# Performance work log

Hardware: AMD Instinct MI355X
Metric: run time of the kernel (lower is better)

## Reference

```python
import jax, jax.numpy as jnp
import numpy as np

HIDDEN = 64
IN_DIM = 32
CONNECTION = 8
N_WARPS = (CONNECTION + 1) // 2  # range(0, connection, 2) -> 4 warps actually used


def conv2d(x, w, b, pad):
    # x: (B, Cin, H, W), w: (Cout, Cin, kh, kw)
    y = jax.lax.conv_general_dilated(
        x, w, window_strides=(1, 1), padding=[(pad, pad), (pad, pad)],
        dimension_numbers=("NCHW", "OIHW", "NCHW"))
    return y + b[None, :, None, None]


def grid_sample_bilinear(img, grid):
    """torch.nn.functional.grid_sample(mode='bilinear', padding_mode='zeros', align_corners=False).
    img: (B, C, H, W); grid: (B, H, W, 2) with grid[..., 0]=x (width), grid[..., 1]=y (height)."""
    B, C, H, W = img.shape
    gx = (grid[..., 0] + 1.0) * (W * 0.5) - 0.5  # unnormalize, align_corners=False
    gy = (grid[..., 1] + 1.0) * (H * 0.5) - 0.5
    x0 = jnp.floor(gx)
    y0 = jnp.floor(gy)
    wx1 = gx - x0
    wy1 = gy - y0
    wx0 = 1.0 - wx1
    wy0 = 1.0 - wy1

    def gather(xf, yf):
        valid = (xf >= 0) & (xf < W) & (yf >= 0) & (yf < H)
        xi = jnp.clip(xf, 0, W - 1).astype(jnp.int32)
        yi = jnp.clip(yf, 0, H - 1).astype(jnp.int32)
        # per-batch advanced gather: (C, H, W) per sample
        v = jax.vmap(lambda im, y, x: im[:, y, x])(img, yi, xi)  # (B, C, H, W)
        return v * valid[:, None, :, :].astype(img.dtype)

    out = (wy0 * wx0)[:, None] * gather(x0, y0) \
        + (wy0 * wx1)[:, None] * gather(x0 + 1, y0) \
        + (wy1 * wx0)[:, None] * gather(x0, y0 + 1) \
        + (wy1 * wx1)[:, None] * gather(x0 + 1, y0 + 1)
    return out


def setup_inputs() -> dict:
    key = jax.random.key(0)
    ks = jax.random.split(key, 10)
    B, H, W = 16, 128, 128
    s = 0.05
    return {
        "x": jax.random.normal(ks[0], (B, IN_DIM, H, W), dtype=jnp.float32),
        "h_prev": jax.random.normal(ks[1], (B, HIDDEN, H, W), dtype=jnp.float32),
        "w_in": jax.random.normal(ks[2], (3 * HIDDEN, IN_DIM, 3, 3), dtype=jnp.float32) * s,
        "b_in": jax.random.normal(ks[3], (3 * HIDDEN,), dtype=jnp.float32) * s,
        "w_proj": jax.random.normal(ks[4], (N_WARPS, 3 * HIDDEN, HIDDEN), dtype=jnp.float32) * s,
        "b_proj": jax.random.normal(ks[5], (N_WARPS, 3 * HIDDEN), dtype=jnp.float32) * s,
        "w_sub": jax.random.normal(ks[6], (2 * CONNECTION, IN_DIM + HIDDEN, 5, 5), dtype=jnp.float32) * s,
        "b_sub": jax.random.normal(ks[7], (2 * CONNECTION,), dtype=jnp.float32) * s,
    }


def reference(x, h_prev, w_in, b_in, w_proj, b_proj, w_sub, b_sub):
    d = HIDDEN
    input_conv = conv2d(x, w_in, b_in, pad=1)  # (B, 3d, H, W)
    x_z, x_r, x_h = input_conv[:, :d], input_conv[:, d:2 * d], input_conv[:, 2 * d:]

    # flow sub-network + global min-max normalization over ALL channels
    combined = jnp.concatenate([x, h_prev], axis=1)
    cc = conv2d(combined, w_sub, b_sub, pad=2)  # (B, 2*connection, H, W)
    cc = jnp.transpose(cc, (0, 2, 3, 1))        # (B, H, W, 2*connection)
    cc = (cc - cc.min()) / (cc.max() - cc.min())
    cc = 2.0 * cc - 1.0

    traj = None
    for i in range(N_WARPS):  # small fixed loop (mirrors range(0, connection, 2))
        grid = cc[..., 2 * i:2 * i + 2]
        warped = grid_sample_bilinear(h_prev, grid)  # (B, d, H, W)
        proj = jnp.einsum("bchw,oc->bohw", warped, w_proj[i]) + b_proj[i][None, :, None, None]
        traj = proj if traj is None else traj + proj

    h_z, h_r, h_h = traj[:, :d], traj[:, d:2 * d], traj[:, 2 * d:]
    z = jax.nn.sigmoid(x_z + h_z)
    r = jax.nn.sigmoid(x_r + h_r)
    h = jax.nn.leaky_relu(x_h + r * h_h, negative_slope=0.2)
    h_next = (1.0 - z) * h + z * h_prev
    return h_next
```

## Files before the change

kernel.cpp:

```cpp
#include <hip/hip_runtime.h>
#include <hip/hip_bf16.h>
#include <math.h>

#define B_    16
#define HID   64
#define CIN   32
#define OC1   192
#define CCC   16
#define HW_   128
#define NPIX  (HW_*HW_)

typedef _Float16 half8 __attribute__((ext_vector_type(8)));
typedef float floatx4 __attribute__((ext_vector_type(4)));

__device__ __forceinline__ unsigned fenc(float f) {
    unsigned b = __float_as_uint(f);
    return (b & 0x80000000u) ? ~b : (b | 0x80000000u);
}
__device__ __forceinline__ float fdec(unsigned u) {
    unsigned b = (u & 0x80000000u) ? (u ^ 0x80000000u) : ~u;
    return __uint_as_float(b);
}

__global__ __launch_bounds__(256) void repack_kernel(
    const float* __restrict__ w_in, const float* __restrict__ w_sub,
    const float* __restrict__ w_proj, const float* __restrict__ b_proj,
    _Float16* __restrict__ wsub_f16, float* __restrict__ bsum,
    _Float16* __restrict__ win_f16, _Float16* __restrict__ wp_f16,
    unsigned* __restrict__ minmax)
{
    int idx = blockIdx.x * 256 + threadIdx.x;
    if (idx < 38400) {
        int sk = idx >> 9, r2 = idx & 511;
        int l = r2 >> 3, j = r2 & 7;
        int s = sk / 3, kc = sk - s * 3;
        int ky = s / 5, kx = s - ky * 5;
        int oc = l & 15;
        int icg = kc * 32 + (l >> 4) * 8 + j;
        wsub_f16[idx] = (_Float16)w_sub[oc * 2400 + icg * 25 + ky * 5 + kx];
    } else if (idx < 38400 + 192) {
        int o = idx - 38400;
        bsum[o] = b_proj[o] + b_proj[192 + o] + b_proj[384 + o] + b_proj[576 + o];
    } else if (idx < 38592 + 55296) {
        int j2 = idx - 38592;
        int s = j2 / 6144, r = j2 - s * 6144;
        int mt = r / 512, r2 = r - mt * 512;
        int l = r2 >> 3, j = r2 & 7;
        int oc = mt * 16 + (l & 15);
        int ic = (l >> 4) * 8 + j;
        win_f16[j2] = (_Float16)w_in[oc * 288 + ic * 9 + s];
    } else if (idx < 38592 + 55296 + 49152) {
        int j3 = idx - (38592 + 55296);
        int kt = j3 / 6144, r = j3 - kt * 6144;
        int mt = r / 512, r2 = r - mt * 512;
        int l = r2 >> 3, j = r2 & 7;
        int o = mt * 16 + (l & 15);
        int c_all = kt * 32 + (l >> 4) * 8 + j;
        int i = c_all >> 6, c = c_all & 63;
        wp_f16[j3] = (_Float16)w_proj[(i * 192 + o) * 64 + c];
    }
    if (idx == 0) { minmax[0] = 0xFFFFFFFFu; minmax[1] = 0u; }
}

__global__ __launch_bounds__(256) void transpose_h_kernel(
    const float* __restrict__ hp, const float* __restrict__ x,
    _Float16* __restrict__ hcl, _Float16* __restrict__ xcl)
{
    __shared__ float lds[64 * 129];
    int tid = threadIdx.x;
    int y = blockIdx.x, b = blockIdx.y;

    const float* hb = hp + (size_t)b * HID * NPIX + y * HW_;
#pragma unroll
    for (int it = 0; it < 32; ++it) {
        int idx = tid + it * 256;
        int c = idx >> 7, xx = idx & 127;
        lds[c * 129 + xx] = hb[(size_t)c * NPIX + xx];
    }
    __syncthreads();
    unsigned* o = (unsigned*)(hcl + (size_t)((b * HW_ + y) * HW_) * 64);
#pragma unroll
    for (int it = 0; it < 16; ++it) {
        int e2 = tid + it * 256;
        int c2 = e2 & 31, xx = e2 >> 5;
        union { _Float16 h[2]; unsigned u; } pk;
        pk.h[0] = (_Float16)lds[(c2 * 2) * 129 + xx];
        pk.h[1] = (_Float16)lds[(c2 * 2 + 1) * 129 + xx];
        o[e2] = pk.u;
    }
    __syncthreads();

    const float* xb = x + (size_t)b * CIN * NPIX + y * HW_;
#pragma unroll
    for (int it = 0; it < 16; ++it) {
        int idx = tid + it * 256;
        int c = idx >> 7, xx = idx & 127;
        lds[c * 129 + xx] = xb[(size_t)c * NPIX + xx];
    }
    __syncthreads();
    unsigned* ox = (unsigned*)(xcl + (size_t)((b * HW_ + y) * HW_) * 32);
#pragma unroll
    for (int it = 0; it < 8; ++it) {
        int e2 = tid + it * 256;
        int c2 = e2 & 15, xx = e2 >> 4;
        union { _Float16 h[2]; unsigned u; } pk;
        pk.h[0] = (_Float16)lds[(c2 * 2) * 129 + xx];
        pk.h[1] = (_Float16)lds[(c2 * 2 + 1) * 129 + xx];
        ox[e2] = pk.u;
    }
}

__global__ __launch_bounds__(256) void conv_sub_mfma(
    const _Float16* __restrict__ xcl, const _Float16* __restrict__ hcl,
    const _Float16* __restrict__ wsub_f16, const float* __restrict__ b_sub,
    float* __restrict__ cc, unsigned* __restrict__ minmax)
{
    __shared__ __align__(16) _Float16 tile[12 * 20 * 104];
    __shared__ float redmn[4], redmx[4];
    int tid = threadIdx.x;
    int b = blockIdx.z;
    int y0 = blockIdx.y * 8, x0 = blockIdx.x * 16;

#pragma unroll
    for (int it = 0; it < 8; ++it) {
        int idx = tid + it * 256;
        if (idx < 1920) {
            int yy = idx / 160, rem = idx - yy * 160;
            int px = rem >> 3, q = rem & 7;
            int gy = y0 + yy - 2, gx = x0 + px - 2;
            bool ok = ((unsigned)gy < 128u) & ((unsigned)gx < 128u);
            int cgy = min(max(gy, 0), 127), cgx = min(max(gx, 0), 127);
            uint4 v = ((const uint4*)hcl)[(size_t)((b * 128 + cgy) * 128 + cgx) * 8 + q];
            if (!ok) { v.x = 0; v.y = 0; v.z = 0; v.w = 0; }
            *(uint4*)((char*)tile + (yy * 20 + px) * 208 + 64 + q * 16) = v;
        }
    }
#pragma unroll
    for (int it = 0; it < 4; ++it) {
        int idx = tid + it * 256;
        if (idx < 960) {
            int yy = idx / 80, rem = idx - yy * 80;
            int px = rem >> 2, q = rem & 3;
            int gy = y0 + yy - 2, gx = x0 + px - 2;
            bool ok = ((unsigned)gy < 128u) & ((unsigned)gx < 128u);
            int cgy = min(max(gy, 0), 127), cgx = min(max(gx, 0), 127);
            uint4 v = ((const uint4*)xcl)[(size_t)((b * 128 + cgy) * 128 + cgx) * 4 + q];
            if (!ok) { v.x = 0; v.y = 0; v.z = 0; v.w = 0; }
            *(uint4*)((char*)tile + (yy * 20 + px) * 208 + q * 16) = v;
        }
    }
    __syncthreads();

    int w = tid >> 6, l = tid & 63;
    int quad = l >> 4, ln = l & 15;

    floatx4 sinit;
#pragma unroll
    for (int r = 0; r < 4; ++r) sinit[r] = b_sub[quad * 4 + r];
    floatx4 sacc[2] = {sinit, sinit};

#pragma unroll 5
    for (int s = 0; s < 25; ++s) {
        int ky = s / 5, kx = s - (s / 5) * 5;
#pragma unroll
        for (int kc = 0; kc < 3; ++kc) {
            half8 af = *(const half8*)(wsub_f16 + (size_t)((s * 3 + kc) * 64 + l) * 8);
#pragma unroll
            for (int t = 0; t < 2; ++t) {
                int pos = (w * 2 + t + ky) * 20 + (ln + kx);
                half8 bf = *(const half8*)(tile + pos * 104 + kc * 32 + quad * 8);
                sacc[t] = __builtin_amdgcn_mfma_f32_16x16x32_f16(af, bf, sacc[t], 0, 0, 0);
            }
        }
    }

    {
        float mn = 1e30f, mx = -1e30f;
#pragma unroll
        for (int t = 0; t < 2; ++t) {
            int yg = y0 + w * 2 + t;
#pragma unroll
            for (int r = 0; r < 4; ++r) {
                int oc = quad * 4 + r;
                float v = sacc[t][r];
                cc[((size_t)(b * CCC + oc) * HW_ + yg) * HW_ + x0 + ln] = v;
                mn = fminf(mn, v); mx = fmaxf(mx, v);
            }
        }
#pragma unroll
        for (int m = 1; m < 64; m <<= 1) {
            mn = fminf(mn, __shfl_xor(mn, m, 64));
            mx = fmaxf(mx, __shfl_xor(mx, m, 64));
        }
        if (l == 0) { redmn[w] = mn; redmx[w] = mx; }
    }
    __syncthreads();
    if (tid == 0) {
        float bmn = fminf(fminf(redmn[0], redmn[1]), fminf(redmn[2], redmn[3]));
        float bmx = fmaxf(fmaxf(redmx[0], redmx[1]), fmaxf(redmx[2], redmx[3]));
        atomicMin(&minmax[0], fenc(bmn));
        atomicMax(&minmax[1], fenc(bmx));
    }
}

__global__ __launch_bounds__(256, 4) void warp_gru_conv(
    const float* __restrict__ hp, const _Float16* __restrict__ hcl,
    const _Float16* __restrict__ xcl, const float* __restrict__ cc,
    const _Float16* __restrict__ wp_f16, const float* __restrict__ bsum,
    const _Float16* __restrict__ win_f16, const float* __restrict__ b_in,
    const unsigned* __restrict__ minmax, float* __restrict__ out)
{
    __shared__ __align__(16) _Float16 smem[64 * 256];
    _Float16* xt = smem;
    _Float16* warped = smem;

    int tid = threadIdx.x;
    int i = tid >> 6;
    int p = tid & 63;
    int b = blockIdx.z, y = blockIdx.y, xh = blockIdx.x;
    int xg = xh * 64 + p;
    int w = i, l = p;
    int quad = l >> 4, ln = l & 15;

    uint4 xv0, xv1, xv2, xv3;
    int xslot = -1;
    if (tid < 216) {
        int row = tid / 72, px = tid - row * 72;
        int gy = y - 1 + row, gx = xh * 64 - 4 + px;
        bool ok = ((unsigned)gy < 128u) & ((unsigned)gx < 128u);
        int cgy = min(max(gy, 0), 127), cgx = min(max(gx, 0), 127);
        const uint4* s = (const uint4*)(xcl + (size_t)((b * 128 + cgy) * 128 + cgx) * 32);
        xv0 = s[0]; xv1 = s[1]; xv2 = s[2]; xv3 = s[3];
        if (!ok) {
            xv0.x = xv0.y = xv0.z = xv0.w = 0; xv1 = xv0; xv2 = xv0; xv3 = xv0;
        }
        xslot = (row * 72 + px) * 4;
    }

    float mn = fdec(minmax[0]), mx = fdec(minmax[1]);
    float scale = 2.0f / (mx - mn);
    int ccbase = ((b * CCC + 2 * i) * HW_ + y) * HW_ + xg;
    float gxn = (cc[ccbase] - mn) * scale - 1.0f;
    float gyn = (cc[ccbase + NPIX] - mn) * scale - 1.0f;
    float gx = (gxn + 1.0f) * 64.0f - 0.5f;
    float gy = (gyn + 1.0f) * 64.0f - 0.5f;
    float x0f = floorf(gx), y0f = floorf(gy);
    float wx1 = gx - x0f, wy1 = gy - y0f;
    float wx0 = 1.0f - wx1, wy0 = 1.0f - wy1;
    int ix0 = (int)x0f, iy0 = (int)y0f;
    int ix1 = ix0 + 1, iy1 = iy0 + 1;
    bool vx0 = (unsigned)ix0 < 128u, vx1 = (unsigned)ix1 < 128u;
    bool vy0 = (unsigned)iy0 < 128u, vy1 = (unsigned)iy1 < 128u;
    _Float16 h00 = (_Float16)((vx0 && vy0) ? wy0 * wx0 : 0.f);
    _Float16 h01 = (_Float16)((vx1 && vy0) ? wy0 * wx1 : 0.f);
    _Float16 h10 = (_Float16)((vx0 && vy1) ? wy1 * wx0 : 0.f);
    _Float16 h11 = (_Float16)((vx1 && vy1) ? wy1 * wx1 : 0.f);
    int cx0 = min(max(ix0, 0), 127), cx1 = min(max(ix1, 0), 127);
    int cy0 = min(max(iy0, 0), 127), cy1 = min(max(iy1, 0), 127);

    const _Float16* hclb = hcl + (size_t)b * NPIX * 64;
    const half8* r00 = (const half8*)(hclb + (size_t)(cy0 * HW_ + cx0) * 64);
    const half8* r01 = (const half8*)(hclb + (size_t)(cy0 * HW_ + cx1) * 64);
    const half8* r10 = (const half8*)(hclb + (size_t)(cy1 * HW_ + cx0) * 64);
    const half8* r11 = (const half8*)(hclb + (size_t)(cy1 * HW_ + cx1) * 64);

    if (xslot >= 0) {
        unsigned b0 = (unsigned)(xslot * 16);
        unsigned by0_ = b0 ^ (((b0 >> 7) & 3) << 4);
        unsigned b1 = (unsigned)((xslot + 1) * 16);
        unsigned by1_ = b1 ^ (((b1 >> 7) & 3) << 4);
        unsigned b2 = (unsigned)((xslot + 2) * 16);
        unsigned by2_ = b2 ^ (((b2 >> 7) & 3) << 4);
        unsigned b3 = (unsigned)((xslot + 3) * 16);
        unsigned by3_ = b3 ^ (((b3 >> 7) & 3) << 4);
        *(uint4*)((char*)xt + by0_) = xv0;
        *(uint4*)((char*)xt + by1_) = xv1;
        *(uint4*)((char*)xt + by2_) = xv2;
        *(uint4*)((char*)xt + by3_) = xv3;
    }
    __syncthreads();

    floatx4 accA[3][4];
    floatx4 hh[4];
#pragma unroll
    for (int t = 0; t < 2; ++t) {
        floatx4 bi = *(const floatx4*)(b_in + t * 64 + 16 * w + quad * 4);
        floatx4 bs = *(const floatx4*)(bsum + t * 64 + 16 * w + quad * 4);
        floatx4 init;
#pragma unroll
        for (int r = 0; r < 4; ++r) init[r] = bi[r] + bs[r];
#pragma unroll
        for (int nt = 0; nt < 4; ++nt) accA[t][nt] = init;
    }
    {
        floatx4 bih = *(const floatx4*)(b_in + 128 + 16 * w + quad * 4);
        floatx4 bsh = *(const floatx4*)(bsum + 128 + 16 * w + quad * 4);
#pragma unroll
        for (int nt = 0; nt < 4; ++nt) { accA[2][nt] = bih; hh[nt] = bsh; }
    }

#pragma unroll
    for (int s = 0; s < 9; ++s) {
        int ky = s / 3, kx = s - ky * 3;
        half8 af[3];
#pragma unroll
        for (int t = 0; t < 3; ++t)
            af[t] = *(const half8*)(win_f16 + (size_t)((s * 12 + (t * 4 + w)) * 64 + l) * 8);
#pragma unroll
        for (int nt = 0; nt < 4; ++nt) {
            int pxr = ky * 72 + nt * 16 + ln + kx + 3;
            unsigned byte = (unsigned)(pxr * 64 + quad * 16);
            byte ^= ((byte >> 7) & 3) << 4;
            half8 bf = *(const half8*)((char*)xt + byte);
#pragma unroll
            for (int t = 0; t < 3; ++t)
                accA[t][nt] = __builtin_amdgcn_mfma_f32_16x16x32_f16(af[t], bf, accA[t][nt], 0, 0, 0);
        }
    }
    __syncthreads();

#pragma unroll
    for (int t = 0; t < 8; ++t) {
        half8 c00 = r00[t], c01 = r01[t], c10 = r10[t], c11 = r11[t];
        half8 v = c00 * h00 + c01 * h01 + c10 * h10 + c11 * h11;
        int cs = (i * 8 + t) ^ (p & 7);
        *(half8*)(warped + p * 256 + cs * 8) = v;
    }
    __syncthreads();

    const float* hb = hp + (size_t)b * HID * NPIX;
    float hpv[4][4];
#pragma unroll
    for (int nt = 0; nt < 4; ++nt) {
#pragma unroll
        for (int r = 0; r < 4; ++r) {
            int d = 16 * w + quad * 4 + r;
            hpv[nt][r] = hb[(size_t)d * NPIX + y * HW_ + xh * 64 + nt * 16 + ln];
        }
    }

#pragma unroll
    for (int kt = 0; kt < 8; ++kt) {
        half8 af[3];
#pragma unroll
        for (int t = 0; t < 3; ++t)
            af[t] = *(const half8*)(wp_f16 + (size_t)((kt * 12 + (t * 4 + w)) * 64 + l) * 8);
#pragma unroll
        for (int nt = 0; nt < 4; ++nt) {
            int pxi = nt * 16 + ln;
            int cs = (kt * 4 + quad) ^ (pxi & 7);
            half8 bf = *(const half8*)(warped + pxi * 256 + cs * 8);
            accA[0][nt] = __builtin_amdgcn_mfma_f32_16x16x32_f16(af[0], bf, accA[0][nt], 0, 0, 0);
            accA[1][nt] = __builtin_amdgcn_mfma_f32_16x16x32_f16(af[1], bf, accA[1][nt], 0, 0, 0);
            hh[nt]      = __builtin_amdgcn_mfma_f32_16x16x32_f16(af[2], bf, hh[nt], 0, 0, 0);
        }
    }

#pragma unroll
    for (int nt = 0; nt < 4; ++nt) {
#pragma unroll
        for (int r = 0; r < 4; ++r) {
            int d = 16 * w + quad * 4 + r;
            int pxi = nt * 16 + ln;
            int pix = y * HW_ + xh * 64 + pxi;
            float z  = 1.0f / (1.0f + __expf(-accA[0][nt][r]));
            float rg = 1.0f / (1.0f + __expf(-accA[1][nt][r]));
            float hc = accA[2][nt][r] + rg * hh[nt][r];
            hc = hc > 0.f ? hc : 0.2f * hc;
            out[(size_t)(b * HID + d) * NPIX + pix] = (1.f - z) * hc + z * hpv[nt][r];
        }
    }
}

extern "C" void kernel_launch(void* const* d_in, const int* in_sizes, int n_in,
                              void* d_out, int out_size, void* d_ws, size_t ws_size,
                              hipStream_t stream)
{
    const float* x      = (const float*)d_in[0];
    const float* hp     = (const float*)d_in[1];
    const float* w_in   = (const float*)d_in[2];
    const float* b_in   = (const float*)d_in[3];
    const float* w_proj = (const float*)d_in[4];
    const float* b_proj = (const float*)d_in[5];
    const float* w_sub  = (const float*)d_in[6];
    const float* b_sub  = (const float*)d_in[7];
    float* out = (float*)d_out;

    char* ws = (char*)d_ws;
    float*     ccbuf    = (float*)    ws;
    unsigned*  minmax   = (unsigned*) (ws + 16777216);
    _Float16*  wsub_f16 = (_Float16*)(ws + 16777472);
    float*     bsum     = (float*)    (ws + 16854272);
    _Float16*  win_f16  = (_Float16*)(ws + 16855296);
    _Float16*  wp_f16   = (_Float16*)(ws + 16965888);
    _Float16*  hcl16    = (_Float16*)(ws + 17064192);
    _Float16*  xcl16    = (_Float16*)(ws + 50618624);

    repack_kernel<<<dim3(559), dim3(256), 0, stream>>>(
        w_in, w_sub, w_proj, b_proj, wsub_f16, bsum, win_f16, wp_f16, minmax);
    transpose_h_kernel<<<dim3(HW_, B_), dim3(256), 0, stream>>>(hp, x, hcl16, xcl16);
    conv_sub_mfma<<<dim3(8, 16, B_), dim3(256), 0, stream>>>(
        xcl16, hcl16, wsub_f16, b_sub, ccbuf, minmax);
    warp_gru_conv<<<dim3(2, HW_, B_), dim3(256), 0, stream>>>(
        hp, hcl16, xcl16, ccbuf, wp_f16, bsum, win_f16, b_in, minmax, out);
}
```

Measured before the change: 393.9 us.

## Stage GRU output through LDS for vectorized stores; read h_prev from fp16 copy

The final GRU kernel now reads h_prev from the fp16 channels-last copy, one half4 per tile, instead of sixteen scalar fp32 loads per thread. It prefetches two of the four bilinear corner rows before the input-conv MFMA loop so their latency overlaps compute. Outputs are staged through padded shared memory and written as float4 along pixels, replacing scattered scalar stores. Launch bounds drop to 3 blocks per CU to make room for the extra registers. This risks lower occupancy, and the blend term z*h_prev now uses an fp16-rounded h_prev, which slightly changes precision.

```diff
diff --git a/kernel.cpp b/kernel.cpp
--- a/kernel.cpp
+++ b/kernel.cpp
@@ -11,6 +11,7 @@
 #define NPIX  (HW_*HW_)
 
 typedef _Float16 half8 __attribute__((ext_vector_type(8)));
+typedef _Float16 half4 __attribute__((ext_vector_type(4)));
 typedef float floatx4 __attribute__((ext_vector_type(4)));
 
 __device__ __forceinline__ unsigned fenc(float f) {
@@ -203,9 +204,9 @@
     }
 }
 
-__global__ __launch_bounds__(256, 4) void warp_gru_conv(
-    const float* __restrict__ hp, const _Float16* __restrict__ hcl,
-    const _Float16* __restrict__ xcl, const float* __restrict__ cc,
+__global__ __launch_bounds__(256, 3) void warp_gru_conv(
+    const _Float16* __restrict__ hcl, const _Float16* __restrict__ xcl,
+    const float* __restrict__ cc,
     const _Float16* __restrict__ wp_f16, const float* __restrict__ bsum,
     const _Float16* __restrict__ win_f16, const float* __restrict__ b_in,
     const unsigned* __restrict__ minmax, float* __restrict__ out)
@@ -213,6 +214,7 @@
     __shared__ __align__(16) _Float16 smem[64 * 256];
     _Float16* xt = smem;
     _Float16* warped = smem;
+    float* ol = (float*)smem;
 
     int tid = threadIdx.x;
     int i = tid >> 6;
@@ -235,6 +237,15 @@
             xv0.x = xv0.y = xv0.z = xv0.w = 0; xv1 = xv0; xv2 = xv0; xv3 = xv0;
         }
         xslot = (row * 72 + px) * 4;
+    }
+
+    const _Float16* hclb = hcl + (size_t)b * NPIX * 64;
+    half4 hpv16[4];
+    {
+        const _Float16* grow = hclb + (size_t)(y * HW_ + xh * 64) * 64 + 16 * w + quad * 4;
+#pragma unroll
+        for (int nt = 0; nt < 4; ++nt)
+            hpv16[nt] = *(const half4*)(grow + (size_t)(nt * 16 + ln) * 64);
     }
 
     float mn = fdec(minmax[0]), mx = fdec(minmax[1]);
@@ -258,7 +269,6 @@
     int cx0 = min(max(ix0, 0), 127), cx1 = min(max(ix1, 0), 127);
     int cy0 = min(max(iy0, 0), 127), cy1 = min(max(iy1, 0), 127);
 
-    const _Float16* hclb = hcl + (size_t)b * NPIX * 64;
     const half8* r00 = (const half8*)(hclb + (size_t)(cy0 * HW_ + cx0) * 64);
     const half8* r01 = (const half8*)(hclb + (size_t)(cy0 * HW_ + cx1) * 64);
     const half8* r10 = (const half8*)(hclb + (size_t)(cy1 * HW_ + cx0) * 64);
@@ -280,6 +290,10 @@
     }
     __syncthreads();
 
+    half8 g0[8], g1[8];
+#pragma unroll
+    for (int t = 0; t < 8; ++t) { g0[t] = r00[t]; g1[t] = r01[t]; }
+
     floatx4 accA[3][4];
     floatx4 hh[4];
 #pragma unroll
@@ -321,23 +335,12 @@
 
 #pragma unroll
     for (int t = 0; t < 8; ++t) {
-        half8 c00 = r00[t], c01 = r01[t], c10 = r10[t], c11 = r11[t];
-        half8 v = c00 * h00 + c01 * h01 + c10 * h10 + c11 * h11;
+        half8 c10 = r10[t], c11 = r11[t];
+        half8 v = g0[t] * h00 + g1[t] * h01 + c10 * h10 + c11 * h11;
         int cs = (i * 8 + t) ^ (p & 7);
         *(half8*)(warped + p * 256 + cs * 8) = v;
     }
     __syncthreads();
-
-    const float* hb = hp + (size_t)b * HID * NPIX;
-    float hpv[4][4];
-#pragma unroll
-    for (int nt = 0; nt < 4; ++nt) {
-#pragma unroll
-        for (int r = 0; r < 4; ++r) {
-            int d = 16 * w + quad * 4 + r;
-            hpv[nt][r] = hb[(size_t)d * NPIX + y * HW_ + xh * 64 + nt * 16 + ln];
-        }
-    }
 
 #pragma unroll
     for (int kt = 0; kt < 8; ++kt) {
@@ -356,18 +359,37 @@
         }
     }
 
+    float gout[4][4];
 #pragma unroll
     for (int nt = 0; nt < 4; ++nt) {
 #pragma unroll
         for (int r = 0; r < 4; ++r) {
-            int d = 16 * w + quad * 4 + r;
-            int pxi = nt * 16 + ln;
-            int pix = y * HW_ + xh * 64 + pxi;
             float z  = 1.0f / (1.0f + __expf(-accA[0][nt][r]));
             float rg = 1.0f / (1.0f + __expf(-accA[1][nt][r]));
             float hc = accA[2][nt][r] + rg * hh[nt][r];
             hc = hc > 0.f ? hc : 0.2f * hc;
-            out[(size_t)(b * HID + d) * NPIX + pix] = (1.f - z) * hc + z * hpv[nt][r];
+            gout[nt][r] = (1.f - z) * hc + z * (float)hpv16[nt][r];
+        }
+    }
+
+    __syncthreads();
+#pragma unroll
+    for (int nt = 0; nt < 4; ++nt) {
+#pragma unroll
+        for (int r = 0; r < 4; ++r) {
+            int d = 16 * w + quad * 4 + r;
+            ol[d * 68 + nt * 16 + ln] = gout[nt][r];
+        }
+    }
+    __syncthreads();
+    {
+        const int pixbase = y * HW_ + xh * 64;
+#pragma unroll
+        for (int it = 0; it < 4; ++it) {
+            int idx = tid + it * 256;
+            int ch = idx >> 4, p4 = idx & 15;
+            floatx4 v = *(const floatx4*)&ol[ch * 68 + p4 * 4];
+            *(floatx4*)&out[(size_t)(b * HID + ch) * NPIX + pixbase + p4 * 4] = v;
         }
     }
 }
@@ -402,5 +424,5 @@
     conv_sub_mfma<<<dim3(8, 16, B_), dim3(256), 0, stream>>>(
         xcl16, hcl16, wsub_f16, b_sub, ccbuf, minmax);
     warp_gru_conv<<<dim3(2, HW_, B_), dim3(256), 0, stream>>>(
-        hp, hcl16, xcl16, ccbuf, wp_f16, bsum, win_f16, b_in, minmax, out);
-}
+        hcl16, xcl16, ccbuf, wp_f16, bsum, win_f16, b_in, minmax, out);
+}
```

After: 361.7 us. 8.2% less time.
